# Kernel optimization log

Hardware: AMD Instinct MI355X
Metric: run time of the kernel (lower is better)

## Reference

```python
import jax, jax.numpy as jnp
import numpy as np

N_DEG = 5
RANK = 4
SCALE = 4
IMW = IMH = 512
S = IMW * IMH
BATCH = 64
C_CH = 1


def setup_inputs() -> dict:
    key = jax.random.key(0)
    k1, k2, k3, k4 = jax.random.split(key, 4)
    x = jax.random.normal(k1, (BATCH, C_CH, IMW // SCALE, IMH // SCALE), dtype=jnp.float32)
    # CP-decomposed polynomial (CCP) factors; small init keeps degree-5 products stable
    A = jax.random.normal(k2, (N_DEG, RANK, S), dtype=jnp.float32) * 0.01
    C = jax.random.normal(k3, (S, RANK), dtype=jnp.float32) * 0.01
    b = jax.random.normal(k4, (S,), dtype=jnp.float32) * 0.01
    return {"x": x, "A": A, "C": C, "b": b}


def reference(x, A, C, b):
    bsize, c, w, h = x.shape
    # bilinear upsample, align_corners=False (half-pixel, matches torch default)
    up = jax.image.resize(x, (bsize, c, w * SCALE, h * SCALE), method="bilinear")
    flat = up.reshape(bsize, c, S)
    v = flat[:, c - 1, :]  # [B, S] -- original applies PolyLayer only to channel c-1
    # CCP polynomial network: z1 = A1 v; z_n = (A_n v) * z_{n-1} + z_{n-1}
    za = jnp.einsum("nrs,bs->bnr", A, v)  # [B, N, rank]
    z = za[:, 0]
    for n in range(1, N_DEG):
        z = za[:, n] * z + z
    out_v = jnp.einsum("br,sr->bs", z, C) + b  # [B, S]
    flat = flat.at[:, c - 1, :].set(out_v)
    return flat.reshape(bsize, c, w * SCALE, h * SCALE)
```

## Files before the change

### kernel.cpp

```cpp
#include <hip/hip_runtime.h>

#define S_TOTAL (512 * 512)
#define BATCH 64
#define KTOT2 16384
#define NPR 16

typedef float vfloat4 __attribute__((ext_vector_type(4)));

__device__ __forceinline__ float swz_x1(float v) {
    return __int_as_float(__builtin_amdgcn_ds_swizzle(__float_as_int(v), 0x041F));
}
__device__ __forceinline__ float swz_x2(float v) {
    return __int_as_float(__builtin_amdgcn_ds_swizzle(__float_as_int(v), 0x081F));
}
__device__ __forceinline__ float swz_x4(float v) {
    return __int_as_float(__builtin_amdgcn_ds_swizzle(__float_as_int(v), 0x101F));
}
__device__ __forceinline__ float swz_x8(float v) {
    return __int_as_float(__builtin_amdgcn_ds_swizzle(__float_as_int(v), 0x201F));
}

__global__ __launch_bounds__(256) void adjxy_kernel(
    const float* __restrict__ A,
    float* __restrict__ B2)
{
    __shared__ float b1loc[20][128];

    const int t  = threadIdx.x;
    const int nr = blockIdx.x >> 5;
    const int tc = blockIdx.x & 31;
    const int y0 = 16 * tc - 2;

    const float* An = A + (size_t)nr * S_TOTAL;

#pragma unroll
    for (int i = t; i < 20 * 128; i += 256) {
        const int rl = i >> 7;
        const int j  = i & 127;
        const int y  = y0 + rl;
        float s = 0.0f;
        if (y >= 0 && y < 512) {
            const float* Ay = An + (size_t)y * 512;
            const int base = 4 * j;
            const vfloat4 m0 = *(const vfloat4*)(Ay + max(base - 4, 0));
            const vfloat4 m1 = *(const vfloat4*)(Ay + base);
            const vfloat4 m2 = *(const vfloat4*)(Ay + min(base + 4, 508));
            float e0 = m0.z, e1 = m0.w, e6 = m2.x, e7 = m2.y;
            if (j == 0)   { e0 = 0.0f; e1 = 0.0f; }
            if (j == 127) { e6 = 0.0f; e7 = 0.0f; }
            s = 0.125f * e0 + 0.375f * e1
              + 0.625f * m1.x + 0.875f * m1.y
              + 0.875f * m1.z + 0.625f * m1.w
              + 0.375f * e6 + 0.125f * e7;
            if (j == 0)   s += 0.375f * Ay[0]   + 0.125f * Ay[1];
            if (j == 127) s += 0.125f * Ay[510] + 0.375f * Ay[511];
        }
        b1loc[rl][j] = s;
    }
    __syncthreads();

    const float w[8] = {0.125f, 0.375f, 0.625f, 0.875f,
                        0.875f, 0.625f, 0.375f, 0.125f};
#pragma unroll
    for (int i = t; i < 512; i += 256) {
        const int tyl = i >> 7;
        const int j   = i & 127;
        const int ty  = tc * 4 + tyl;
        float s = 0.0f;
#pragma unroll
        for (int p = 0; p < 8; ++p)
            s = fmaf(w[p], b1loc[4 * tyl + p][j], s);
        if (ty == 0)   s += 0.375f * b1loc[2][j]  + 0.125f * b1loc[3][j];
        if (ty == 127) s += 0.125f * b1loc[16][j] + 0.375f * b1loc[17][j];
        B2[(size_t)nr * KTOT2 + ty * 128 + j] = s;
    }
}

__global__ __launch_bounds__(512) void za_partial_kernel(
    const float* __restrict__ x,
    const float* __restrict__ B2,
    float* __restrict__ partial)
{
    __shared__ float red[4][80];

    const int t    = threadIdx.x;
    const int kc4  = blockIdx.x >> 4;
    const int bqn  = blockIdx.x & 15;
    const int wv   = t >> 6;
    const int lane = t & 63;
    const int kcl  = wv & 3;
    const int bh   = wv >> 2;
    const int kc   = kc4 * 4 + kcl;
    const int b0   = bqn * 4 + bh * 2;
    const size_t kbase = (size_t)kc * 256 + 4 * lane;

    const vfloat4 xv0 = *(const vfloat4*)(x + (size_t)b0 * KTOT2 + kbase);
    const vfloat4 xv1 = *(const vfloat4*)(x + (size_t)(b0 + 1) * KTOT2 + kbase);

    const int lane1 = lane & 1, lane2 = lane & 2;

#pragma unroll
    for (int ch = 0; ch < 2; ++ch) {
        float acc[4][5];
#pragma unroll
        for (int v = 0; v < 4; ++v)
#pragma unroll
            for (int tt = 0; tt < 5; ++tt) acc[v][tt] = 0.0f;

#pragma unroll
        for (int tt = 0; tt < 5; ++tt)
#pragma unroll
            for (int par = 0; par < 2; ++par) {
                const int nr = ch * 10 + 2 * tt + par;
                const vfloat4 bq4 = *(const vfloat4*)(B2 + (size_t)nr * KTOT2 + kbase);
                acc[par][tt] =
                    fmaf(bq4.x, xv0.x, fmaf(bq4.y, xv0.y,
                    fmaf(bq4.z, xv0.z, fmaf(bq4.w, xv0.w, acc[par][tt]))));
                acc[2 + par][tt] =
                    fmaf(bq4.x, xv1.x, fmaf(bq4.y, xv1.y,
                    fmaf(bq4.z, xv1.z, fmaf(bq4.w, xv1.w, acc[2 + par][tt]))));
            }

        float s1[2][5];
#pragma unroll
        for (int v = 0; v < 2; ++v)
#pragma unroll
            for (int tt = 0; tt < 5; ++tt) {
                const float u = acc[v][tt], h = acc[v + 2][tt];
                s1[v][tt] = (lane1 ? h : u) + swz_x1(lane1 ? u : h);
            }
        float s2[5];
#pragma unroll
        for (int tt = 0; tt < 5; ++tt) {
            const float u = s1[0][tt], h = s1[1][tt];
            s2[tt] = (lane2 ? h : u) + swz_x2(lane2 ? u : h);
        }
#pragma unroll
        for (int tt = 0; tt < 5; ++tt) {
            s2[tt] += swz_x4(s2[tt]);
            s2[tt] += swz_x8(s2[tt]);
            s2[tt] += __shfl_xor(s2[tt], 16, 64);
            s2[tt] += __shfl_xor(s2[tt], 32, 64);
        }

        if (lane < 4) {
            const int bi  = lane & 1;
            const int par = (lane >> 1) & 1;
#pragma unroll
            for (int tt = 0; tt < 5; ++tt)
                red[kcl][(bh * 2 + bi) * 20 + ch * 10 + 2 * tt + par] = s2[tt];
        }
    }

    __syncthreads();
    if (t < 80) {
        const float s = red[0][t] + red[1][t] + red[2][t] + red[3][t];
        const int bl = t / 20;
        const int nr = t - bl * 20;
        partial[(size_t)kc4 * 1280 + (bqn * 4 + bl) * 20 + nr] = s;
    }
}

__global__ __launch_bounds__(256) void out_kernel(
    const float* __restrict__ C,
    const float* __restrict__ bias,
    const float* __restrict__ partial,
    float* __restrict__ out)
{
    __shared__ float za_sh[1280];
    __shared__ float zs[256];
    const int t = threadIdx.x;

    const int sb = blockIdx.x >> 1;
    const int bh = blockIdx.x & 1;
    const int s0 = (sb * 256 + t) * 4;
    const vfloat4 c0 = *(const vfloat4*)(C + (size_t)s0 * 4);
    const vfloat4 c1 = *(const vfloat4*)(C + (size_t)s0 * 4 + 4);
    const vfloat4 c2 = *(const vfloat4*)(C + (size_t)s0 * 4 + 8);
    const vfloat4 c3 = *(const vfloat4*)(C + (size_t)s0 * 4 + 12);
    const vfloat4 bv = *(const vfloat4*)(bias + s0);

#pragma unroll
    for (int q = 0; q < 5; ++q) {
        const int c = q * 256 + t;
        float a0 = 0, a1 = 0, a2 = 0, a3 = 0;
#pragma unroll
        for (int r = 0; r < NPR; r += 4) {
            a0 += partial[(size_t)(r + 0) * 1280 + c];
            a1 += partial[(size_t)(r + 1) * 1280 + c];
            a2 += partial[(size_t)(r + 2) * 1280 + c];
            a3 += partial[(size_t)(r + 3) * 1280 + c];
        }
        za_sh[c] = (a0 + a1) + (a2 + a3);
    }
    __syncthreads();
    if (t < 64) {
#pragma unroll
        for (int r = 0; r < 4; ++r) {
            float zv = za_sh[t * 20 + r];
#pragma unroll
            for (int n = 1; n < 5; ++n)
                zv *= (1.0f + za_sh[t * 20 + n * 4 + r]);
            zs[t * 4 + r] = zv;
        }
    }
    __syncthreads();

#pragma unroll 8
    for (int bb = bh * 32; bb < bh * 32 + 32; ++bb) {
        const float z0 = zs[bb * 4 + 0], z1 = zs[bb * 4 + 1];
        const float z2 = zs[bb * 4 + 2], z3 = zs[bb * 4 + 3];
        vfloat4 o;
        o.x = fmaf(z0, c0.x, fmaf(z1, c0.y, fmaf(z2, c0.z, fmaf(z3, c0.w, bv.x))));
        o.y = fmaf(z0, c1.x, fmaf(z1, c1.y, fmaf(z2, c1.z, fmaf(z3, c1.w, bv.y))));
        o.z = fmaf(z0, c2.x, fmaf(z1, c2.y, fmaf(z2, c2.z, fmaf(z3, c2.w, bv.z))));
        o.w = fmaf(z0, c3.x, fmaf(z1, c3.y, fmaf(z2, c3.z, fmaf(z3, c3.w, bv.w))));
        __builtin_nontemporal_store(o, (vfloat4*)(out + (size_t)bb * S_TOTAL + s0));
    }
}

extern "C" void kernel_launch(void* const* d_in, const int* in_sizes, int n_in,
                              void* d_out, int out_size, void* d_ws, size_t ws_size,
                              hipStream_t stream)
{
    const float* x    = (const float*)d_in[0];
    const float* A    = (const float*)d_in[1];
    const float* C    = (const float*)d_in[2];
    const float* bias = (const float*)d_in[3];
    float* out = (float*)d_out;

    float* B2      = (float*)d_ws;
    float* partial = B2 + (size_t)20 * KTOT2;

    adjxy_kernel<<<640, 256, 0, stream>>>(A, B2);
    za_partial_kernel<<<256, 512, 0, stream>>>(x, B2, partial);
    out_kernel<<<512, 256, 0, stream>>>(C, bias, partial, out);
}
```

Baseline: 33.27 us.

## Fuse A-downsampling and x contraction into one kernel, dropping B2 round trip

Merges the kernel that folds the bilinear adjoint into A (producing B2) with the kernel that contracts B2 against x. Each block now computes an 8-row tile of B2 for one (n,r) in shared memory and immediately dots it with all 64 batch rows of x, writing per-tile partials. This removes one launch and the global write/read of B2, at the cost of each block rereading the x tile (x is reloaded by 20 blocks) and larger shared memory per block.

```diff
diff --git a/kernel.cpp b/kernel.cpp
--- a/kernel.cpp
+++ b/kernel.cpp
@@ -2,7 +2,6 @@
 
 #define S_TOTAL (512 * 512)
 #define BATCH 64
-#define KTOT2 16384
 #define NPR 16
 
 typedef float vfloat4 __attribute__((ext_vector_type(4)));
@@ -20,21 +19,25 @@
     return __int_as_float(__builtin_amdgcn_ds_swizzle(__float_as_int(v), 0x201F));
 }
 
-__global__ __launch_bounds__(256) void adjxy_kernel(
+__global__ __launch_bounds__(512) void fused_za_kernel(
+    const float* __restrict__ x,
     const float* __restrict__ A,
-    float* __restrict__ B2)
+    float* __restrict__ partial)
 {
-    __shared__ float b1loc[20][128];
-
-    const int t  = threadIdx.x;
-    const int nr = blockIdx.x >> 5;
-    const int tc = blockIdx.x & 31;
-    const int y0 = 16 * tc - 2;
+    __shared__ float b1loc[36][128];
+    __shared__ float b2loc[1024];
+
+    const int t   = threadIdx.x;
+    const int blk = blockIdx.x;
+    const int q   = blk >> 3;
+    const int nr  = q % 20;
+    const int tcp = (q / 20) * 8 + (blk & 7);
+    const int y0  = 32 * tcp - 2;
 
     const float* An = A + (size_t)nr * S_TOTAL;
 
-#pragma unroll
-    for (int i = t; i < 20 * 128; i += 256) {
+#pragma unroll 3
+    for (int i = t; i < 36 * 128; i += 512) {
         const int rl = i >> 7;
         const int j  = i & 127;
         const int y  = y0 + rl;
@@ -62,102 +65,71 @@
     const float w[8] = {0.125f, 0.375f, 0.625f, 0.875f,
                         0.875f, 0.625f, 0.375f, 0.125f};
 #pragma unroll
-    for (int i = t; i < 512; i += 256) {
+    for (int i = t; i < 1024; i += 512) {
         const int tyl = i >> 7;
         const int j   = i & 127;
-        const int ty  = tc * 4 + tyl;
+        const int ty  = tcp * 8 + tyl;
         float s = 0.0f;
 #pragma unroll
         for (int p = 0; p < 8; ++p)
             s = fmaf(w[p], b1loc[4 * tyl + p][j], s);
         if (ty == 0)   s += 0.375f * b1loc[2][j]  + 0.125f * b1loc[3][j];
-        if (ty == 127) s += 0.125f * b1loc[16][j] + 0.375f * b1loc[17][j];
-        B2[(size_t)nr * KTOT2 + ty * 128 + j] = s;
-    }
-}
-
-__global__ __launch_bounds__(512) void za_partial_kernel(
-    const float* __restrict__ x,
-    const float* __restrict__ B2,
-    float* __restrict__ partial)
-{
-    __shared__ float red[4][80];
-
-    const int t    = threadIdx.x;
-    const int kc4  = blockIdx.x >> 4;
-    const int bqn  = blockIdx.x & 15;
+        if (ty == 127) s += 0.125f * b1loc[32][j] + 0.375f * b1loc[33][j];
+        b2loc[i] = s;
+    }
+    __syncthreads();
+
     const int wv   = t >> 6;
     const int lane = t & 63;
-    const int kcl  = wv & 3;
-    const int bh   = wv >> 2;
-    const int kc   = kc4 * 4 + kcl;
-    const int b0   = bqn * 4 + bh * 2;
-    const size_t kbase = (size_t)kc * 256 + 4 * lane;
-
-    const vfloat4 xv0 = *(const vfloat4*)(x + (size_t)b0 * KTOT2 + kbase);
-    const vfloat4 xv1 = *(const vfloat4*)(x + (size_t)(b0 + 1) * KTOT2 + kbase);
-
-    const int lane1 = lane & 1, lane2 = lane & 2;
-
-#pragma unroll
-    for (int ch = 0; ch < 2; ++ch) {
-        float acc[4][5];
-#pragma unroll
-        for (int v = 0; v < 4; ++v)
-#pragma unroll
-            for (int tt = 0; tt < 5; ++tt) acc[v][tt] = 0.0f;
-
-#pragma unroll
-        for (int tt = 0; tt < 5; ++tt)
-#pragma unroll
-            for (int par = 0; par < 2; ++par) {
-                const int nr = ch * 10 + 2 * tt + par;
-                const vfloat4 bq4 = *(const vfloat4*)(B2 + (size_t)nr * KTOT2 + kbase);
-                acc[par][tt] =
-                    fmaf(bq4.x, xv0.x, fmaf(bq4.y, xv0.y,
-                    fmaf(bq4.z, xv0.z, fmaf(bq4.w, xv0.w, acc[par][tt]))));
-                acc[2 + par][tt] =
-                    fmaf(bq4.x, xv1.x, fmaf(bq4.y, xv1.y,
-                    fmaf(bq4.z, xv1.z, fmaf(bq4.w, xv1.w, acc[2 + par][tt]))));
-            }
-
-        float s1[2][5];
-#pragma unroll
-        for (int v = 0; v < 2; ++v)
-#pragma unroll
-            for (int tt = 0; tt < 5; ++tt) {
-                const float u = acc[v][tt], h = acc[v + 2][tt];
-                s1[v][tt] = (lane1 ? h : u) + swz_x1(lane1 ? u : h);
-            }
-        float s2[5];
-#pragma unroll
-        for (int tt = 0; tt < 5; ++tt) {
-            const float u = s1[0][tt], h = s1[1][tt];
-            s2[tt] = (lane2 ? h : u) + swz_x2(lane2 ? u : h);
-        }
-#pragma unroll
-        for (int tt = 0; tt < 5; ++tt) {
-            s2[tt] += swz_x4(s2[tt]);
-            s2[tt] += swz_x8(s2[tt]);
-            s2[tt] += __shfl_xor(s2[tt], 16, 64);
-            s2[tt] += __shfl_xor(s2[tt], 32, 64);
-        }
-
-        if (lane < 4) {
-            const int bi  = lane & 1;
-            const int par = (lane >> 1) & 1;
-#pragma unroll
-            for (int tt = 0; tt < 5; ++tt)
-                red[kcl][(bh * 2 + bi) * 20 + ch * 10 + 2 * tt + par] = s2[tt];
-        }
-    }
-
-    __syncthreads();
-    if (t < 80) {
-        const float s = red[0][t] + red[1][t] + red[2][t] + red[3][t];
-        const int bl = t / 20;
-        const int nr = t - bl * 20;
-        partial[(size_t)kc4 * 1280 + (bqn * 4 + bl) * 20 + nr] = s;
+    const int b0   = wv * 8;
+    const size_t xbase = (size_t)tcp * 1024 + 4 * lane;
+
+    vfloat4 bq0 = *(const vfloat4*)&b2loc[4 * lane];
+    vfloat4 bq1 = *(const vfloat4*)&b2loc[4 * lane + 256];
+    vfloat4 bq2 = *(const vfloat4*)&b2loc[4 * lane + 512];
+    vfloat4 bq3 = *(const vfloat4*)&b2loc[4 * lane + 768];
+
+    float acc[8];
+#pragma unroll
+    for (int bi = 0; bi < 8; ++bi) {
+        const float* xb = x + (size_t)(b0 + bi) * 16384 + xbase;
+        const vfloat4 x0 = *(const vfloat4*)(xb);
+        const vfloat4 x1 = *(const vfloat4*)(xb + 256);
+        const vfloat4 x2 = *(const vfloat4*)(xb + 512);
+        const vfloat4 x3 = *(const vfloat4*)(xb + 768);
+        float a = 0.0f;
+        a = fmaf(bq0.x, x0.x, fmaf(bq0.y, x0.y, fmaf(bq0.z, x0.z, fmaf(bq0.w, x0.w, a))));
+        a = fmaf(bq1.x, x1.x, fmaf(bq1.y, x1.y, fmaf(bq1.z, x1.z, fmaf(bq1.w, x1.w, a))));
+        a = fmaf(bq2.x, x2.x, fmaf(bq2.y, x2.y, fmaf(bq2.z, x2.z, fmaf(bq2.w, x2.w, a))));
+        a = fmaf(bq3.x, x3.x, fmaf(bq3.y, x3.y, fmaf(bq3.z, x3.z, fmaf(bq3.w, x3.w, a))));
+        acc[bi] = a;
+    }
+
+    const int lane1 = lane & 1, lane2 = lane & 2, lane4 = lane & 4;
+    float s1[4];
+#pragma unroll
+    for (int v = 0; v < 4; ++v) {
+        const float u = acc[v], h = acc[v + 4];
+        s1[v] = (lane1 ? h : u) + swz_x1(lane1 ? u : h);
+    }
+    float s2[2];
+#pragma unroll
+    for (int v = 0; v < 2; ++v) {
+        const float u = s1[v], h = s1[v + 2];
+        s2[v] = (lane2 ? h : u) + swz_x2(lane2 ? u : h);
+    }
+    float s3;
+    {
+        const float u = s2[0], h = s2[1];
+        s3 = (lane4 ? h : u) + swz_x4(lane4 ? u : h);
+    }
+    s3 += swz_x8(s3);
+    s3 += __shfl_xor(s3, 16, 64);
+    s3 += __shfl_xor(s3, 32, 64);
+
+    if (lane < 8) {
+        const int m = ((lane & 1) << 2) | (lane & 2) | ((lane & 4) >> 2);
+        partial[(size_t)tcp * 1280 + (b0 + m) * 20 + nr] = s3;
     }
 }
 
@@ -181,8 +153,8 @@
     const vfloat4 bv = *(const vfloat4*)(bias + s0);
 
 #pragma unroll
-    for (int q = 0; q < 5; ++q) {
-        const int c = q * 256 + t;
+    for (int qq = 0; qq < 5; ++qq) {
+        const int c = qq * 256 + t;
         float a0 = 0, a1 = 0, a2 = 0, a3 = 0;
 #pragma unroll
         for (int r = 0; r < NPR; r += 4) {
@@ -229,10 +201,8 @@
     const float* bias = (const float*)d_in[3];
     float* out = (float*)d_out;
 
-    float* B2      = (float*)d_ws;
-    float* partial = B2 + (size_t)20 * KTOT2;
-
-    adjxy_kernel<<<640, 256, 0, stream>>>(A, B2);
-    za_partial_kernel<<<256, 512, 0, stream>>>(x, B2, partial);
+    float* partial = (float*)d_ws;
+
+    fused_za_kernel<<<320, 512, 0, stream>>>(x, A, partial);
     out_kernel<<<512, 256, 0, stream>>>(C, bias, partial, out);
 }
```

Result: faster. 31.11 us, median of 2 (-6.5%).
